# Optimization experiments

Hardware: AMD Instinct MI355X
Metric: run time of the kernel (lower is better)

Reference implementation:

```python
import jax, jax.numpy as jnp
import numpy as np

N = 8192
SIZE = 32  # output_dimension


def setup_inputs() -> dict:
    key = jax.random.key(0)
    k1, k2, k3, k4, k5 = jax.random.split(key, 5)
    previous_inclusion_score = jax.random.normal(k1, (N,), dtype=jnp.float32)
    nodes = jax.random.normal(k2, (N, 3), dtype=jnp.float32)
    adjacency_matrix = jax.random.randint(k3, (N, N), 0, 2, dtype=jnp.int32)
    W_phi = jax.random.normal(k4, (SIZE,), dtype=jnp.float32)
    W_theta = jax.random.normal(k5, (3, 1), dtype=jnp.float32)
    return {
        "previous_inclusion_score": previous_inclusion_score,
        "nodes": nodes,
        "adjacency_matrix": adjacency_matrix,
        "W_phi": W_phi,
        "W_theta": W_theta,
    }


def reference(previous_inclusion_score, nodes, adjacency_matrix, W_phi, W_theta):
    # Per node i: max over neighbors j of || w * (x_i - x_j) ||_2, w = W_theta[:,0].
    # ||w*(x_i - x_j)||^2 = |y_i|^2 + |y_j|^2 - 2 y_i.y_j with y = w * x, so we
    # never materialize the [N,N,3] diff tensor.
    w = W_theta[:, 0]                      # [3]
    y = nodes * w[None, :]                 # [N,3] scaled coords
    sq = jnp.sum(y * y, axis=1)            # [N]
    gram = y @ y.T                         # [N,N]
    d2 = sq[:, None] + sq[None, :] - 2.0 * gram   # [N,N] squared weighted dists
    d2 = jnp.where(adjacency_matrix > 0, d2, -jnp.inf)
    max_dist = jnp.sqrt(jnp.maximum(jnp.max(d2, axis=1), 0.0))  # [N]
    inc_score = max_dist[:, None] * W_phi[None, :]              # [N, SIZE]
    # previous_inclusion_score is non-empty and SIZE != 1 -> mean over features,
    # then average with the previous score.
    inc_mean = jnp.mean(inc_score, axis=1)                      # [N]
    return (previous_inclusion_score + inc_mean) * 0.5
```

## Files before the change

### kernel.cpp

```cpp
#include <hip/hip_runtime.h>
#include <math.h>

#define NN 8192
#define NPHI 32
#define ROWS 4
#define TPB 256

typedef int iv4 __attribute__((ext_vector_type(4)));

__global__ void prep_kernel(const float* __restrict__ nodes,
                            const float* __restrict__ W_theta,
                            float4* __restrict__ linear,
                            float4* __restrict__ perm) {
    int j = blockIdx.x * blockDim.x + threadIdx.x;
    if (j >= NN) return;
    float w0 = W_theta[0], w1 = W_theta[1], w2 = W_theta[2];
    float y0 = nodes[3 * j + 0] * w0;
    float y1 = nodes[3 * j + 1] * w1;
    float y2 = nodes[3 * j + 2] * w2;
    float sq = y0 * y0 + y1 * y1 + y2 * y2;
    float4 v = make_float4(y0, y1, y2, sq);
    linear[j] = v;
    perm[(j & ~255) + 64 * (j & 3) + ((j & 255) >> 2)] = v;
}

__launch_bounds__(TPB, 8)
__global__ void maxdist_kernel(const float* __restrict__ prev,
                               const int* __restrict__ adj,
                               const float* __restrict__ W_phi,
                               const float4* __restrict__ linear,
                               const float4* __restrict__ perm,
                               float* __restrict__ out) {
    const int tid  = threadIdx.x;
    const int lane = tid & 63;
    const int wave = tid >> 6;
    const int i0   = blockIdx.x * ROWS;

    float a[ROWS], b[ROWS], c[ROWS], m[ROWS];
#pragma unroll
    for (int r = 0; r < ROWS; ++r) {
        float4 p = linear[i0 + r];
        a[r] = -2.0f * p.x;
        b[r] = -2.0f * p.y;
        c[r] = -2.0f * p.z;
        m[r] = -INFINITY;
    }

    const int iters = NN / 1024;

    for (int k = 0; k < iters; ++k) {
        const int cb = k * 1024 + wave * 256;
        const int j0 = cb + lane * 4;

        iv4 av[ROWS];
#pragma unroll
        for (int r = 0; r < ROWS; ++r)
            av[r] = *(const iv4*)(adj + (size_t)(i0 + r) * NN + j0);

        float4 p[4];
#pragma unroll
        for (int t = 0; t < 4; ++t) p[t] = perm[cb + 64 * t + lane];

#pragma unroll
        for (int r = 0; r < ROWS; ++r) {
#pragma unroll
            for (int t = 0; t < 4; ++t) {
                float d2 = fmaf(a[r], p[t].x,
                            fmaf(b[r], p[t].y,
                             fmaf(c[r], p[t].z, p[t].w)));
                d2 = (av[r][t] > 0) ? d2 : -INFINITY;
                m[r] = fmaxf(m[r], d2);
            }
        }
    }

#pragma unroll
    for (int r = 0; r < ROWS; ++r) {
        float v = m[r];
#pragma unroll
        for (int off = 32; off > 0; off >>= 1)
            v = fmaxf(v, __shfl_xor(v, off, 64));
        m[r] = v;
    }

    __shared__ float red[4][ROWS];
    if (lane == 0) {
#pragma unroll
        for (int r = 0; r < ROWS; ++r) red[wave][r] = m[r];
    }

    float wp = (lane < NPHI) ? W_phi[lane] : 0.0f;
#pragma unroll
    for (int off = 32; off > 0; off >>= 1) wp += __shfl_xor(wp, off, 64);
    const float wmean = wp / (float)NPHI;

    __syncthreads();

    if (tid < ROWS) {
        const int r = tid;
        const float d2max = fmaxf(fmaxf(red[0][r], red[1][r]),
                                  fmaxf(red[2][r], red[3][r]));
        const int i = i0 + r;
        const float si = linear[i].w;
        float d2 = si + d2max;
        d2 = fmaxf(d2, 0.0f);
        const float md = sqrtf(d2);
        out[i] = (prev[i] + md * wmean) * 0.5f;
    }
}

extern "C" void kernel_launch(void* const* d_in, const int* in_sizes, int n_in,
                              void* d_out, int out_size, void* d_ws, size_t ws_size,
                              hipStream_t stream) {
    const float* prev    = (const float*)d_in[0];
    const float* nodes   = (const float*)d_in[1];
    const int*   adj     = (const int*)d_in[2];
    const float* W_phi   = (const float*)d_in[3];
    const float* W_theta = (const float*)d_in[4];
    float* out = (float*)d_out;

    float4* linear = (float4*)d_ws;
    float4* perm   = (float4*)d_ws + NN;

    prep_kernel<<<(NN + TPB - 1) / TPB, TPB, 0, stream>>>(nodes, W_theta, linear, perm);

    maxdist_kernel<<<NN / ROWS, TPB, 0, stream>>>(prev, adj, W_phi, linear, perm, out);
}
```

Measured before the change: 53.37 us.

## Stage adjacency rows into LDS via async global_load_lds double buffering

```diff
diff --git a/kernel.cpp b/kernel.cpp
--- a/kernel.cpp
+++ b/kernel.cpp
@@ -1,12 +1,12 @@
 #include <hip/hip_runtime.h>
 #include <math.h>
 
-#define NN 8192
-#define NPHI 32
-#define ROWS 4
-#define TPB 256
-
-typedef int iv4 __attribute__((ext_vector_type(4)));
+#define NN    8192
+#define NPHI  32
+#define ROWS  4
+#define TPB   256
+#define W     512
+#define TILES (NN / W)
 
 __global__ void prep_kernel(const float* __restrict__ nodes,
                             const float* __restrict__ W_theta,
@@ -21,7 +21,7 @@
     float sq = y0 * y0 + y1 * y1 + y2 * y2;
     float4 v = make_float4(y0, y1, y2, sq);
     linear[j] = v;
-    perm[(j & ~255) + 64 * (j & 3) + ((j & 255) >> 2)] = v;
+    perm[(j & ~127) + 64 * (j & 1) + ((j & 127) >> 1)] = v;
 }
 
 __launch_bounds__(TPB, 8)
@@ -36,6 +36,9 @@
     const int wave = tid >> 6;
     const int i0   = blockIdx.x * ROWS;
 
+    __shared__ int   ladj[2][ROWS * W];
+    __shared__ float red[4][ROWS];
+
     float a[ROWS], b[ROWS], c[ROWS], m[ROWS];
 #pragma unroll
     for (int r = 0; r < ROWS; ++r) {
@@ -46,32 +49,43 @@
         m[r] = -INFINITY;
     }
 
-    const int iters = NN / 1024;
+    const int* rowbase = adj + (size_t)(i0 + wave) * NN;
+    auto stage = [&](int buf, int tile) {
+#pragma unroll
+        for (int h = 0; h < 2; ++h) {
+            const int* src = rowbase + tile * W + h * 256 + lane * 4;
+            int* dst = &ladj[buf][wave * W + h * 256];
+            __builtin_amdgcn_global_load_lds(
+                (const __attribute__((address_space(1))) int*)src,
+                (__attribute__((address_space(3))) int*)dst, 16, 0, 0);
+        }
+    };
 
-    for (int k = 0; k < iters; ++k) {
-        const int cb = k * 1024 + wave * 256;
-        const int j0 = cb + lane * 4;
+    stage(0, 0);
+    __syncthreads();
 
-        iv4 av[ROWS];
-#pragma unroll
-        for (int r = 0; r < ROWS; ++r)
-            av[r] = *(const iv4*)(adj + (size_t)(i0 + r) * NN + j0);
+    for (int t = 0; t < TILES; ++t) {
+        const int buf = t & 1;
+        if (t + 1 < TILES) stage(buf ^ 1, t + 1);
+        __syncthreads();
 
-        float4 p[4];
-#pragma unroll
-        for (int t = 0; t < 4; ++t) p[t] = perm[cb + 64 * t + lane];
+        const int qb = t * W + wave * 128;
+        const int lq = wave * 128 + 2 * lane;
+
+        float4 p0 = perm[qb + lane];
+        float4 p1 = perm[qb + 64 + lane];
 
 #pragma unroll
         for (int r = 0; r < ROWS; ++r) {
-#pragma unroll
-            for (int t = 0; t < 4; ++t) {
-                float d2 = fmaf(a[r], p[t].x,
-                            fmaf(b[r], p[t].y,
-                             fmaf(c[r], p[t].z, p[t].w)));
-                d2 = (av[r][t] > 0) ? d2 : -INFINITY;
-                m[r] = fmaxf(m[r], d2);
-            }
+            const int2 ad = *(const int2*)&ladj[buf][r * W + lq];
+            float d20 = fmaf(a[r], p0.x, fmaf(b[r], p0.y, fmaf(c[r], p0.z, p0.w)));
+            float d21 = fmaf(a[r], p1.x, fmaf(b[r], p1.y, fmaf(c[r], p1.z, p1.w)));
+            d20 = (ad.x > 0) ? d20 : -INFINITY;
+            d21 = (ad.y > 0) ? d21 : -INFINITY;
+            m[r] = fmaxf(m[r], fmaxf(d20, d21));
         }
+
+        __syncthreads();
     }
 
 #pragma unroll
@@ -83,7 +97,6 @@
         m[r] = v;
     }
 
-    __shared__ float red[4][ROWS];
     if (lane == 0) {
 #pragma unroll
         for (int r = 0; r < ROWS; ++r) red[wave][r] = m[r];
```

Result: faster. 51.67 us (-3.2%).

## Fuse prep into maxdist kernel, recompute scaled coords on the fly

Applied to the files above, without the earlier changes.

```diff
diff --git a/kernel.cpp b/kernel.cpp
--- a/kernel.cpp
+++ b/kernel.cpp
@@ -1,77 +1,76 @@
 #include <hip/hip_runtime.h>
 #include <math.h>
 
-#define NN 8192
+#define NN   8192
 #define NPHI 32
-#define ROWS 4
-#define TPB 256
+#define ROWS 2
+#define TPB  256
 
 typedef int iv4 __attribute__((ext_vector_type(4)));
 
-__global__ void prep_kernel(const float* __restrict__ nodes,
-                            const float* __restrict__ W_theta,
-                            float4* __restrict__ linear,
-                            float4* __restrict__ perm) {
-    int j = blockIdx.x * blockDim.x + threadIdx.x;
-    if (j >= NN) return;
-    float w0 = W_theta[0], w1 = W_theta[1], w2 = W_theta[2];
-    float y0 = nodes[3 * j + 0] * w0;
-    float y1 = nodes[3 * j + 1] * w1;
-    float y2 = nodes[3 * j + 2] * w2;
-    float sq = y0 * y0 + y1 * y1 + y2 * y2;
-    float4 v = make_float4(y0, y1, y2, sq);
-    linear[j] = v;
-    perm[(j & ~255) + 64 * (j & 3) + ((j & 255) >> 2)] = v;
-}
-
 __launch_bounds__(TPB, 8)
 __global__ void maxdist_kernel(const float* __restrict__ prev,
+                               const float* __restrict__ nodes,
                                const int* __restrict__ adj,
                                const float* __restrict__ W_phi,
-                               const float4* __restrict__ linear,
-                               const float4* __restrict__ perm,
+                               const float* __restrict__ W_theta,
                                float* __restrict__ out) {
     const int tid  = threadIdx.x;
     const int lane = tid & 63;
     const int wave = tid >> 6;
     const int i0   = blockIdx.x * ROWS;
 
+    const float w0 = W_theta[0], w1 = W_theta[1], w2 = W_theta[2];
+
     float a[ROWS], b[ROWS], c[ROWS], m[ROWS];
 #pragma unroll
     for (int r = 0; r < ROWS; ++r) {
-        float4 p = linear[i0 + r];
-        a[r] = -2.0f * p.x;
-        b[r] = -2.0f * p.y;
-        c[r] = -2.0f * p.z;
+        const float yi0 = nodes[3 * (i0 + r) + 0] * w0;
+        const float yi1 = nodes[3 * (i0 + r) + 1] * w1;
+        const float yi2 = nodes[3 * (i0 + r) + 2] * w2;
+        a[r] = -2.0f * yi0;
+        b[r] = -2.0f * yi1;
+        c[r] = -2.0f * yi2;
         m[r] = -INFINITY;
     }
 
-    const int iters = NN / 1024;
+    const int woff = wave * 256 + lane * 4;
 
-    for (int k = 0; k < iters; ++k) {
-        const int cb = k * 1024 + wave * 256;
-        const int j0 = cb + lane * 4;
-
-        iv4 av[ROWS];
+    auto consume = [&](const iv4* av, int jbase) {
+        const float4* nb = (const float4*)(nodes + 3 * jbase);
+        const float4 q0 = nb[0], q1 = nb[1], q2 = nb[2];
+        const float nf[12] = {q0.x, q0.y, q0.z, q0.w,
+                              q1.x, q1.y, q1.z, q1.w,
+                              q2.x, q2.y, q2.z, q2.w};
 #pragma unroll
-        for (int r = 0; r < ROWS; ++r)
-            av[r] = *(const iv4*)(adj + (size_t)(i0 + r) * NN + j0);
-
-        float4 p[4];
+        for (int t = 0; t < 4; ++t) {
+            const float y0 = nf[3 * t + 0] * w0;
+            const float y1 = nf[3 * t + 1] * w1;
+            const float y2 = nf[3 * t + 2] * w2;
+            const float sq = fmaf(y0, y0, fmaf(y1, y1, y2 * y2));
 #pragma unroll
-        for (int t = 0; t < 4; ++t) p[t] = perm[cb + 64 * t + lane];
-
-#pragma unroll
-        for (int r = 0; r < ROWS; ++r) {
-#pragma unroll
-            for (int t = 0; t < 4; ++t) {
-                float d2 = fmaf(a[r], p[t].x,
-                            fmaf(b[r], p[t].y,
-                             fmaf(c[r], p[t].z, p[t].w)));
+            for (int r = 0; r < ROWS; ++r) {
+                float d2 = fmaf(a[r], y0, fmaf(b[r], y1, fmaf(c[r], y2, sq)));
                 d2 = (av[r][t] > 0) ? d2 : -INFINITY;
                 m[r] = fmaxf(m[r], d2);
             }
         }
+    };
+
+    for (int k = 0; k < NN / 1024; k += 2) {
+        const int j00 = k * 1024 + woff;
+        const int j01 = j00 + 1024;
+
+        iv4 av0[ROWS], av1[ROWS];
+#pragma unroll
+        for (int r = 0; r < ROWS; ++r)
+            av0[r] = *(const iv4*)(adj + (size_t)(i0 + r) * NN + j00);
+#pragma unroll
+        for (int r = 0; r < ROWS; ++r)
+            av1[r] = *(const iv4*)(adj + (size_t)(i0 + r) * NN + j01);
+
+        consume(av0, j00);
+        consume(av1, j01);
     }
 
 #pragma unroll
@@ -101,7 +100,10 @@
         const float d2max = fmaxf(fmaxf(red[0][r], red[1][r]),
                                   fmaxf(red[2][r], red[3][r]));
         const int i = i0 + r;
-        const float si = linear[i].w;
+        const float yi0 = nodes[3 * i + 0] * w0;
+        const float yi1 = nodes[3 * i + 1] * w1;
+        const float yi2 = nodes[3 * i + 2] * w2;
+        const float si  = fmaf(yi0, yi0, fmaf(yi1, yi1, yi2 * yi2));
         float d2 = si + d2max;
         d2 = fmaxf(d2, 0.0f);
         const float md = sqrtf(d2);
@@ -119,10 +121,5 @@
     const float* W_theta = (const float*)d_in[4];
     float* out = (float*)d_out;
 
-    float4* linear = (float4*)d_ws;
-    float4* perm   = (float4*)d_ws + NN;
-
-    prep_kernel<<<(NN + TPB - 1) / TPB, TPB, 0, stream>>>(nodes, W_theta, linear, perm);
-
-    maxdist_kernel<<<NN / ROWS, TPB, 0, stream>>>(prev, adj, W_phi, linear, perm, out);
+    maxdist_kernel<<<NN / ROWS, TPB, 0, stream>>>(prev, nodes, adj, W_phi, W_theta, out);
 }
```

Result: faster. 45.47 us (median of 2 runs) (-14.8%).
